# Kernel optimization log

Measured on AMD Instinct MI355X. Metric: run time of the kernel, lower is better.

The kernel has to match this reference:

```python
import jax, jax.numpy as jnp
import numpy as np

WD, WH, WW = 2, 7, 7
N = WD * WH * WW          # 98 tokens per window
DIM = 128
HEADS = 4
HEAD_DIM = DIM // HEADS   # 32
B_ = 2048                 # num_windows * batch
NW = 64                   # windows per image (mask leading dim)
TABLE = (2 * WD - 1) * (2 * WH - 1) * (2 * WW - 1)  # 507


def _relative_position_index():
    coords = np.stack(np.meshgrid(np.arange(WD), np.arange(WH), np.arange(WW), indexing='ij'))
    flat = coords.reshape(3, -1)                     # [3, N]
    rel = flat[:, :, None] - flat[:, None, :]        # [3, N, N]
    rel = rel.transpose(1, 2, 0).copy()              # [N, N, 3]
    rel[:, :, 0] += WD - 1
    rel[:, :, 1] += WH - 1
    rel[:, :, 2] += WW - 1
    rel[:, :, 0] *= (2 * WH - 1) * (2 * WW - 1)
    rel[:, :, 1] *= 2 * WW - 1
    return rel.sum(-1).astype(np.int32)             # [N, N]


def setup_inputs() -> dict:
    key = jax.random.key(0)
    ks = jax.random.split(key, 6)
    x = jax.random.normal(ks[0], (B_, N, DIM), dtype=jnp.float32)
    mask = jax.random.normal(ks[1], (NW, N, N), dtype=jnp.float32)
    qkv_w = jax.random.normal(ks[2], (3 * DIM, DIM), dtype=jnp.float32) * 0.02
    qkv_b = jnp.zeros((3 * DIM,), dtype=jnp.float32)
    proj_w = jax.random.normal(ks[3], (DIM, DIM), dtype=jnp.float32) * 0.02
    proj_b = jnp.zeros((DIM,), dtype=jnp.float32)
    bias_table = jax.random.normal(ks[4], (TABLE, HEADS), dtype=jnp.float32) * 0.02
    rel_idx = jnp.asarray(_relative_position_index())
    return {"x": x, "mask": mask, "qkv_w": qkv_w, "qkv_b": qkv_b,
            "proj_w": proj_w, "proj_b": proj_b, "bias_table": bias_table,
            "rel_idx": rel_idx}


def reference(x, mask, qkv_w, qkv_b, proj_w, proj_b, bias_table, rel_idx):
    b, n, c = x.shape
    hd = c // HEADS
    scale = hd ** -0.5
    qkv = x @ qkv_w.T + qkv_b                          # [B_, N, 3C]
    qkv = qkv.reshape(b, n, 3, HEADS, hd)
    qkv = jnp.transpose(qkv, (2, 0, 3, 1, 4))          # [3, B_, H, N, hd]
    q, k, v = qkv[0], qkv[1], qkv[2]
    attn = jnp.einsum('bhnd,bhmd->bhnm', q * scale, k)  # [B_, H, N, N]
    # gathered relative position bias
    bias = bias_table[rel_idx.reshape(-1)].reshape(n, n, HEADS)
    bias = jnp.transpose(bias, (2, 0, 1))               # [H, N, N]
    attn = attn + bias[None]
    nw = mask.shape[0]
    attn = attn.reshape(b // nw, nw, HEADS, n, n) + mask[None, :, None]
    attn = jax.nn.softmax(attn.reshape(b, HEADS, n, n), axis=-1)
    out = jnp.einsum('bhnm,bhmd->bnhd', attn, v).reshape(b, n, c)
    out = out @ proj_w.T + proj_b
    return out
```

## Files before the change

### kernel.cpp

```cpp
#include <hip/hip_runtime.h>
#include <stdint.h>

#define NTOK 98
#define DIM 128
#define HEADS 4
#define HD 32
#define BWIN 2048
#define NW 64
#define SCALE 0.17677669529663687f
#define QSTR 40
#define VSTR 104

typedef __bf16 bf16_t;
typedef bf16_t bf16x8 __attribute__((ext_vector_type(8)));
typedef float f32x4 __attribute__((ext_vector_type(4)));
typedef unsigned short u16;
typedef unsigned int u32;
typedef unsigned long long u64;

__device__ __forceinline__ u16 f2bf(float f) {
    union { bf16_t h; u16 u; } v; v.h = (bf16_t)f; return v.u;
}
__device__ __forceinline__ float bf2f(u16 b) {
    union { u16 u; bf16_t h; } v; v.u = b; return (float)v.h;
}

__global__ void k0_prep(const float* __restrict__ qkv_w, const float* __restrict__ proj_w,
                        const float* __restrict__ mask,
                        const float* __restrict__ bias_table, const int* __restrict__ rel_idx,
                        u16* __restrict__ qkvw_bf, u16* __restrict__ pw_bf,
                        u16* __restrict__ mbT)
{
    int t = blockIdx.x * 256 + threadIdx.x;
    if (t < 49152) {
        qkvw_bf[t] = f2bf(qkv_w[t]);
    } else if (t < 65536) {
        int r = t - 49152;
        pw_bf[r] = f2bf(proj_w[r]);
    } else {
        int r = t - 65536;
        int w    = r / 50176;
        int rem  = r - w * 50176;
        int hh   = rem / 12544;
        int rem2 = rem - hh * 12544;
        int i    = rem2 >> 7;
        int c    = rem2 & 127;
        int l16  = c >> 3;
        int njp  = c & 7;
        int j    = njp * 16 + l16;
        float val = 0.f;
        if (njp < 7 && j < NTOK)
            val = mask[w * 9604 + i * NTOK + j] + bias_table[rel_idx[i * NTOK + j] * HEADS + hh];
        mbT[r] = f2bf(val);
    }
}

__global__ __launch_bounds__(512, 2) void k_fused(
    const float* __restrict__ x, const u16* __restrict__ qkvw_bf,
    const float* __restrict__ qkv_b, const u16* __restrict__ mbT,
    const u16* __restrict__ pw_bf, const float* __restrict__ proj_b,
    float* __restrict__ out)
{
    __shared__ __align__(16) u16 XO[98 * 136];
    __shared__ __align__(16) u16 qLs[HEADS][98 * QSTR];
    __shared__ __align__(16) u16 kLs[HEADS][98 * QSTR];
    __shared__ __align__(16) u16 vLs[HEADS][HD * VSTR];
    __shared__ __align__(16) u16 Pscr[8][16 * VSTR];
    __shared__ float qkvb_l[384];
    __shared__ float projb_l[128];

    const int b    = blockIdx.x;
    const int tid  = threadIdx.x;
    const int wave = tid >> 6;
    const int lane = tid & 63;
    const int l16  = lane & 15;
    const int quad = lane >> 4;

    if (tid < 384) qkvb_l[tid] = qkv_b[tid];
    else projb_l[tid - 384] = proj_b[tid - 384];

    const float* xb = x + (size_t)b * (NTOK * DIM);
    for (int idx = tid; idx < (NTOK * DIM / 4); idx += 512) {
        int row = idx >> 5;
        int c4  = idx & 31;
        const float4 v = reinterpret_cast<const float4*>(xb)[idx];
        u64 pack = (u64)f2bf(v.x) | ((u64)f2bf(v.y) << 16) |
                   ((u64)f2bf(v.z) << 32) | ((u64)f2bf(v.w) << 48);
        *reinterpret_cast<u64*>(&XO[row * 136 + c4 * 4]) = pack;
    }
    __syncthreads();

    {
        const int u0 = wave * 3 - ((wave > 5) ? (wave - 5) : 0);
        const int u1 = u0 + ((wave < 5) ? 3 : 2);
        for (int np = 0; np < 4; ++np) {
            int cached = -1;
            bf16x8 Bf[2][4];
            for (int u = u0; u < u1; ++u) {
                const int part = u / 7;
                const int mt   = u - part * 7;
                if (part != cached) {
                    const u16* wp = qkvw_bf + (size_t)part * DIM * DIM;
#pragma unroll
                    for (int half = 0; half < 2; ++half)
#pragma unroll
                        for (int ks = 0; ks < 4; ++ks)
                            Bf[half][ks] = *reinterpret_cast<const bf16x8*>(
                                wp + ((np * 2 + half) * 16 + l16) * DIM + quad * 8 + ks * 32);
                    cached = part;
                }
                int arow = mt * 16 + l16;
                if (arow > 97) arow = 97;
                f32x4 acc0 = {0.f, 0.f, 0.f, 0.f};
                f32x4 acc1 = {0.f, 0.f, 0.f, 0.f};
#pragma unroll
                for (int ks = 0; ks < 4; ++ks) {
                    bf16x8 a = *reinterpret_cast<const bf16x8*>(
                        &XO[arow * 136 + quad * 8 + ks * 32]);
                    acc0 = __builtin_amdgcn_mfma_f32_16x16x32_bf16(a, Bf[0][ks], acc0, 0, 0, 0);
                    acc1 = __builtin_amdgcn_mfma_f32_16x16x32_bf16(a, Bf[1][ks], acc1, 0, 0, 0);
                }
                const int tokb = mt * 16 + quad * 4;
#pragma unroll
                for (int half = 0; half < 2; ++half) {
                    const f32x4& acc = half ? acc1 : acc0;
                    int col = (np * 2 + half) * 16 + l16;
                    int h   = col >> 5;
                    int d   = col & 31;
                    float cb = qkvb_l[part * DIM + col];
                    if (part == 0) {
#pragma unroll
                        for (int reg = 0; reg < 4; ++reg) {
                            int tok = tokb + reg;
                            if (tok < NTOK)
                                qLs[h][tok * QSTR + d] = f2bf((acc[reg] + cb) * SCALE);
                        }
                    } else if (part == 1) {
#pragma unroll
                        for (int reg = 0; reg < 4; ++reg) {
                            int tok = tokb + reg;
                            if (tok < NTOK)
                                kLs[h][tok * QSTR + d] = f2bf(acc[reg] + cb);
                        }
                    } else {
                        u16* vrow = &vLs[h][d * VSTR];
                        if (tokb + 3 <= 97) {
                            u64 pack = 0;
#pragma unroll
                            for (int reg = 0; reg < 4; ++reg)
                                pack |= ((u64)f2bf(acc[reg] + cb)) << (16 * reg);
                            *reinterpret_cast<u64*>(&vrow[tokb]) = pack;
                        } else if (tokb <= 97) {
                            u32 pack = (u32)f2bf(acc[0] + cb) | ((u32)f2bf(acc[1] + cb) << 16);
                            *reinterpret_cast<u32*>(&vrow[tokb]) = pack;
                        }
                    }
                }
            }
        }
    }
    __syncthreads();

    {
        const int h   = wave >> 1;
        const int mlo = (wave & 1) ? 4 : 0;
        const int mhi = (wave & 1) ? 7 : 4;
        const u16* qh  = &qLs[h][0];
        const u16* kh  = &kLs[h][0];
        const u16* vh  = &vLs[h][0];
        const u16* mbtp = mbT + ((size_t)((b & (NW - 1)) * HEADS + h)) * (NTOK * 128);
        u16* ps = &Pscr[wave][0];

        bf16x8 kf[7];
#pragma unroll
        for (int nj = 0; nj < 7; ++nj)
            kf[nj] = *reinterpret_cast<const bf16x8*>(&kh[(nj * 16 + l16) * QSTR + quad * 8]);

        for (int mt = mlo; mt < mhi; ++mt) {
            bf16x8 mrows[4];
#pragma unroll
            for (int reg = 0; reg < 4; ++reg) {
                int i  = mt * 16 + quad * 4 + reg;
                int ic = (i > 97) ? 97 : i;
                mrows[reg] = *reinterpret_cast<const bf16x8*>(&mbtp[ic * 128 + l16 * 8]);
            }
            bf16x8 qf = *reinterpret_cast<const bf16x8*>(&qh[(mt * 16 + l16) * QSTR + quad * 8]);
            f32x4 sacc[7];
#pragma unroll
            for (int nj = 0; nj < 7; ++nj) {
                f32x4 z = {0.f, 0.f, 0.f, 0.f};
                sacc[nj] = __builtin_amdgcn_mfma_f32_16x16x32_bf16(qf, kf[nj], z, 0, 0, 0);
            }
#pragma unroll
            for (int reg = 0; reg < 4; ++reg) {
                int i = mt * 16 + quad * 4 + reg;
                bool irow = (i < NTOK);
                float s[7];
#pragma unroll
                for (int nj = 0; nj < 7; ++nj) {
                    int j = nj * 16 + l16;
                    float val = -1e30f;
                    if (irow && j < NTOK)
                        val = sacc[nj][reg] + (float)mrows[reg][nj];
                    s[nj] = val;
                }
                float mx = s[0];
#pragma unroll
                for (int nj = 1; nj < 7; ++nj) mx = fmaxf(mx, s[nj]);
#pragma unroll
                for (int off = 1; off < 16; off <<= 1) mx = fmaxf(mx, __shfl_xor(mx, off));
                float p[7];
                float lsum = 0.f;
#pragma unroll
                for (int nj = 0; nj < 7; ++nj) {
                    float pv = (s[nj] > -1e29f) ? __expf(s[nj] - mx) : 0.f;
                    p[nj] = pv;
                    lsum += pv;
                }
#pragma unroll
                for (int off = 1; off < 16; off <<= 1) lsum += __shfl_xor(lsum, off);
                float rinv = 1.f / ((lsum > 0.f) ? lsum : 1.f);
#pragma unroll
                for (int nj = 0; nj < 7; ++nj) {
                    int j = nj * 16 + l16;
                    if (irow && j < NTOK)
                        ps[(quad * 4 + reg) * VSTR + j] = f2bf(p[nj] * rinv);
                }
            }
            bf16x8 pf[3];
#pragma unroll
            for (int ks = 0; ks < 3; ++ks)
                pf[ks] = *reinterpret_cast<const bf16x8*>(&ps[l16 * VSTR + quad * 8 + ks * 32]);
#pragma unroll
            for (int nt = 0; nt < 2; ++nt) {
                f32x4 oacc = {0.f, 0.f, 0.f, 0.f};
#pragma unroll
                for (int ks = 0; ks < 3; ++ks) {
                    bf16x8 vf = *reinterpret_cast<const bf16x8*>(
                        &vh[(nt * 16 + l16) * VSTR + quad * 8 + ks * 32]);
                    oacc = __builtin_amdgcn_mfma_f32_16x16x32_bf16(pf[ks], vf, oacc, 0, 0, 0);
                }
                int d = nt * 16 + l16;
                float v96 = bf2f(vh[d * VSTR + 96]);
                float v97 = bf2f(vh[d * VSTR + 97]);
#pragma unroll
                for (int reg = 0; reg < 4; ++reg) {
                    int i = mt * 16 + quad * 4 + reg;
                    if (i < NTOK) {
                        float p96 = bf2f(ps[(quad * 4 + reg) * VSTR + 96]);
                        float p97 = bf2f(ps[(quad * 4 + reg) * VSTR + 97]);
                        XO[i * 136 + h * HD + d] = f2bf(oacc[reg] + p96 * v96 + p97 * v97);
                    }
                }
            }
        }
    }
    __syncthreads();

    {
        const int nt = wave;
        bf16x8 bw[4];
#pragma unroll
        for (int ks = 0; ks < 4; ++ks)
            bw[ks] = *reinterpret_cast<const bf16x8*>(
                pw_bf + (nt * 16 + l16) * DIM + quad * 8 + ks * 32);
        const int col = nt * 16 + l16;
        const float pb = projb_l[col];
        for (int mt = 0; mt < 7; ++mt) {
            int arow = mt * 16 + l16;
            if (arow > 97) arow = 97;
            f32x4 acc = {0.f, 0.f, 0.f, 0.f};
#pragma unroll
            for (int ks = 0; ks < 4; ++ks) {
                bf16x8 a = *reinterpret_cast<const bf16x8*>(
                    &XO[arow * 136 + quad * 8 + ks * 32]);
                acc = __builtin_amdgcn_mfma_f32_16x16x32_bf16(a, bw[ks], acc, 0, 0, 0);
            }
#pragma unroll
            for (int reg = 0; reg < 4; ++reg) {
                int row = mt * 16 + quad * 4 + reg;
                if (row < NTOK)
                    out[((size_t)b * NTOK + row) * DIM + col] = acc[reg] + pb;
            }
        }
    }
}

extern "C" void kernel_launch(void* const* d_in, const int* in_sizes, int n_in,
                              void* d_out, int out_size, void* d_ws, size_t ws_size,
                              hipStream_t stream)
{
    const float* x       = (const float*)d_in[0];
    const float* mask    = (const float*)d_in[1];
    const float* qkv_w   = (const float*)d_in[2];
    const float* qkv_b   = (const float*)d_in[3];
    const float* proj_w  = (const float*)d_in[4];
    const float* proj_b  = (const float*)d_in[5];
    const float* bias_tb = (const float*)d_in[6];
    const int*   rel_idx = (const int*)d_in[7];
    float* out = (float*)d_out;

    char* ws = (char*)d_ws;
    u16* qkvw_bf = (u16*)(ws + 0);
    u16* pw_bf   = (u16*)(ws + 98304);
    u16* mbT     = (u16*)(ws + 131072);

    k0_prep<<<12800, 256, 0, stream>>>(qkv_w, proj_w, mask, bias_tb, rel_idx,
                                       qkvw_bf, pw_bf, mbT);
    k_fused<<<BWIN, 512, 0, stream>>>(x, qkvw_bf, qkv_b, mbT, pw_bf, proj_b, out);
}
```

Baseline: 403.9 us.

## Split fused window attention into per-head attention kernel plus separate projection kernel

The single per-window kernel is replaced by a per-(window, head) attention kernel with 256 threads and smaller shared memory. It reads x directly from global memory, converts it to bf16 in registers, and writes the bf16 head outputs to a workspace buffer. A second kernel then performs the output projection. The aim is higher occupancy and more blocks in flight. The cost is that x is re-read once per head and there is an extra global round trip for the attention output.

```diff
diff --git a/kernel.cpp b/kernel.cpp
--- a/kernel.cpp
+++ b/kernel.cpp
@@ -55,20 +55,204 @@
     }
 }
 
-__global__ __launch_bounds__(512, 2) void k_fused(
+__global__ __launch_bounds__(256, 4) void k_attn(
     const float* __restrict__ x, const u16* __restrict__ qkvw_bf,
     const float* __restrict__ qkv_b, const u16* __restrict__ mbT,
-    const u16* __restrict__ pw_bf, const float* __restrict__ proj_b,
-    float* __restrict__ out)
+    u16* __restrict__ OG)
 {
-    __shared__ __align__(16) u16 XO[98 * 136];
-    __shared__ __align__(16) u16 qLs[HEADS][98 * QSTR];
-    __shared__ __align__(16) u16 kLs[HEADS][98 * QSTR];
-    __shared__ __align__(16) u16 vLs[HEADS][HD * VSTR];
-    __shared__ __align__(16) u16 Pscr[8][16 * VSTR];
-    __shared__ float qkvb_l[384];
-    __shared__ float projb_l[128];
-
+    __shared__ __align__(16) u16 qL[NTOK * QSTR];
+    __shared__ __align__(16) u16 kL[NTOK * QSTR];
+    __shared__ __align__(16) u16 vL[HD * VSTR];
+    __shared__ __align__(16) u16 Pscr[4][16 * VSTR];
+
+    const int bh   = (blockIdx.x & 7) * 1024 + (blockIdx.x >> 3);
+    const int b    = bh >> 2;
+    const int h    = bh & 3;
+    const int tid  = threadIdx.x;
+    const int wave = tid >> 6;
+    const int lane = tid & 63;
+    const int l16  = lane & 15;
+    const int quad = lane >> 4;
+
+    const float* xb = x + (size_t)b * (NTOK * DIM);
+
+    {
+        const int u0 = (wave * 21) >> 2;
+        const int u1 = ((wave + 1) * 21) >> 2;
+        int cached = -1;
+        bf16x8 Bf[2][4];
+        float  cb[2];
+        for (int u = u0; u < u1; ++u) {
+            const int part = u / 7;
+            const int mt   = u - part * 7;
+            if (part != cached) {
+                const u16* wp = qkvw_bf + (size_t)part * DIM * DIM;
+#pragma unroll
+                for (int nt2 = 0; nt2 < 2; ++nt2) {
+                    const int col = h * HD + nt2 * 16 + l16;
+#pragma unroll
+                    for (int ks = 0; ks < 4; ++ks)
+                        Bf[nt2][ks] = *reinterpret_cast<const bf16x8*>(
+                            wp + col * DIM + quad * 8 + ks * 32);
+                    cb[nt2] = qkv_b[part * DIM + col];
+                }
+                cached = part;
+            }
+            int arow = mt * 16 + l16;
+            if (arow > 97) arow = 97;
+            bf16x8 af[4];
+#pragma unroll
+            for (int ks = 0; ks < 4; ++ks) {
+                const float* xr = xb + arow * DIM + quad * 8 + ks * 32;
+                const float4 a0 = *reinterpret_cast<const float4*>(xr);
+                const float4 a1 = *reinterpret_cast<const float4*>(xr + 4);
+                bf16x8 a;
+                a[0] = (bf16_t)a0.x; a[1] = (bf16_t)a0.y; a[2] = (bf16_t)a0.z; a[3] = (bf16_t)a0.w;
+                a[4] = (bf16_t)a1.x; a[5] = (bf16_t)a1.y; a[6] = (bf16_t)a1.z; a[7] = (bf16_t)a1.w;
+                af[ks] = a;
+            }
+            f32x4 acc0 = {0.f, 0.f, 0.f, 0.f};
+            f32x4 acc1 = {0.f, 0.f, 0.f, 0.f};
+#pragma unroll
+            for (int ks = 0; ks < 4; ++ks) {
+                acc0 = __builtin_amdgcn_mfma_f32_16x16x32_bf16(af[ks], Bf[0][ks], acc0, 0, 0, 0);
+                acc1 = __builtin_amdgcn_mfma_f32_16x16x32_bf16(af[ks], Bf[1][ks], acc1, 0, 0, 0);
+            }
+            const int tokb = mt * 16 + quad * 4;
+#pragma unroll
+            for (int nt2 = 0; nt2 < 2; ++nt2) {
+                const f32x4& acc = nt2 ? acc1 : acc0;
+                const int d = nt2 * 16 + l16;
+                const float cbv = cb[nt2];
+                if (part == 0) {
+#pragma unroll
+                    for (int reg = 0; reg < 4; ++reg) {
+                        int tok = tokb + reg;
+                        if (tok < NTOK)
+                            qL[tok * QSTR + d] = f2bf((acc[reg] + cbv) * SCALE);
+                    }
+                } else if (part == 1) {
+#pragma unroll
+                    for (int reg = 0; reg < 4; ++reg) {
+                        int tok = tokb + reg;
+                        if (tok < NTOK)
+                            kL[tok * QSTR + d] = f2bf(acc[reg] + cbv);
+                    }
+                } else {
+                    u16* vrow = &vL[d * VSTR];
+                    if (tokb + 3 <= 97) {
+                        u64 pack = 0;
+#pragma unroll
+                        for (int reg = 0; reg < 4; ++reg)
+                            pack |= ((u64)f2bf(acc[reg] + cbv)) << (16 * reg);
+                        *reinterpret_cast<u64*>(&vrow[tokb]) = pack;
+                    } else if (tokb <= 97) {
+                        u32 pack = (u32)f2bf(acc[0] + cbv) | ((u32)f2bf(acc[1] + cbv) << 16);
+                        *reinterpret_cast<u32*>(&vrow[tokb]) = pack;
+                    }
+                }
+            }
+        }
+    }
+    __syncthreads();
+
+    {
+        const u16* mbtp = mbT + ((size_t)((b & (NW - 1)) * HEADS + h)) * (NTOK * 128);
+        u16* ps = &Pscr[wave][0];
+
+        bf16x8 kf[7];
+#pragma unroll
+        for (int nj = 0; nj < 7; ++nj)
+            kf[nj] = *reinterpret_cast<const bf16x8*>(&kL[(nj * 16 + l16) * QSTR + quad * 8]);
+
+        for (int mi = 0; mi < 2; ++mi) {
+            const int mt = wave + mi * 4;
+            if (mt > 6) break;
+            bf16x8 mrows[4];
+#pragma unroll
+            for (int reg = 0; reg < 4; ++reg) {
+                int i  = mt * 16 + quad * 4 + reg;
+                int ic = (i > 97) ? 97 : i;
+                mrows[reg] = *reinterpret_cast<const bf16x8*>(&mbtp[ic * 128 + l16 * 8]);
+            }
+            bf16x8 qf = *reinterpret_cast<const bf16x8*>(&qL[(mt * 16 + l16) * QSTR + quad * 8]);
+            f32x4 sacc[7];
+#pragma unroll
+            for (int nj = 0; nj < 7; ++nj) {
+                f32x4 z = {0.f, 0.f, 0.f, 0.f};
+                sacc[nj] = __builtin_amdgcn_mfma_f32_16x16x32_bf16(qf, kf[nj], z, 0, 0, 0);
+            }
+#pragma unroll
+            for (int reg = 0; reg < 4; ++reg) {
+                int i = mt * 16 + quad * 4 + reg;
+                bool irow = (i < NTOK);
+                float s[7];
+#pragma unroll
+                for (int nj = 0; nj < 7; ++nj) {
+                    int j = nj * 16 + l16;
+                    float val = -1e30f;
+                    if (irow && j < NTOK)
+                        val = sacc[nj][reg] + (float)mrows[reg][nj];
+                    s[nj] = val;
+                }
+                float mx = s[0];
+#pragma unroll
+                for (int nj = 1; nj < 7; ++nj) mx = fmaxf(mx, s[nj]);
+#pragma unroll
+                for (int off = 1; off < 16; off <<= 1) mx = fmaxf(mx, __shfl_xor(mx, off));
+                float p[7];
+                float lsum = 0.f;
+#pragma unroll
+                for (int nj = 0; nj < 7; ++nj) {
+                    float pv = (s[nj] > -1e29f) ? __expf(s[nj] - mx) : 0.f;
+                    p[nj] = pv;
+                    lsum += pv;
+                }
+#pragma unroll
+                for (int off = 1; off < 16; off <<= 1) lsum += __shfl_xor(lsum, off);
+                float rinv = 1.f / ((lsum > 0.f) ? lsum : 1.f);
+#pragma unroll
+                for (int nj = 0; nj < 7; ++nj) {
+                    int j = nj * 16 + l16;
+                    if (irow && j < NTOK)
+                        ps[(quad * 4 + reg) * VSTR + j] = f2bf(p[nj] * rinv);
+                }
+            }
+            bf16x8 pf[3];
+#pragma unroll
+            for (int ks = 0; ks < 3; ++ks)
+                pf[ks] = *reinterpret_cast<const bf16x8*>(&ps[l16 * VSTR + quad * 8 + ks * 32]);
+#pragma unroll
+            for (int nt = 0; nt < 2; ++nt) {
+                f32x4 oacc = {0.f, 0.f, 0.f, 0.f};
+#pragma unroll
+                for (int ks = 0; ks < 3; ++ks) {
+                    bf16x8 vf = *reinterpret_cast<const bf16x8*>(
+                        &vL[(nt * 16 + l16) * VSTR + quad * 8 + ks * 32]);
+                    oacc = __builtin_amdgcn_mfma_f32_16x16x32_bf16(pf[ks], vf, oacc, 0, 0, 0);
+                }
+                int d = nt * 16 + l16;
+                float v96 = bf2f(vL[d * VSTR + 96]);
+                float v97 = bf2f(vL[d * VSTR + 97]);
+#pragma unroll
+                for (int reg = 0; reg < 4; ++reg) {
+                    int i = mt * 16 + quad * 4 + reg;
+                    if (i < NTOK) {
+                        float p96 = bf2f(ps[(quad * 4 + reg) * VSTR + 96]);
+                        float p97 = bf2f(ps[(quad * 4 + reg) * VSTR + 97]);
+                        OG[((size_t)b * NTOK + i) * DIM + h * HD + d] =
+                            f2bf(oacc[reg] + p96 * v96 + p97 * v97);
+                    }
+                }
+            }
+        }
+    }
+}
+
+__global__ __launch_bounds__(256, 4) void k_proj(
+    const u16* __restrict__ OG, const u16* __restrict__ pw_bf,
+    const float* __restrict__ proj_b, float* __restrict__ out)
+{
     const int b    = blockIdx.x;
     const int tid  = threadIdx.x;
     const int wave = tid >> 6;
@@ -76,211 +260,41 @@
     const int l16  = lane & 15;
     const int quad = lane >> 4;
 
-    if (tid < 384) qkvb_l[tid] = qkv_b[tid];
-    else projb_l[tid - 384] = proj_b[tid - 384];
-
-    const float* xb = x + (size_t)b * (NTOK * DIM);
-    for (int idx = tid; idx < (NTOK * DIM / 4); idx += 512) {
-        int row = idx >> 5;
-        int c4  = idx & 31;
-        const float4 v = reinterpret_cast<const float4*>(xb)[idx];
-        u64 pack = (u64)f2bf(v.x) | ((u64)f2bf(v.y) << 16) |
-                   ((u64)f2bf(v.z) << 32) | ((u64)f2bf(v.w) << 48);
-        *reinterpret_cast<u64*>(&XO[row * 136 + c4 * 4]) = pack;
-    }
-    __syncthreads();
-
-    {
-        const int u0 = wave * 3 - ((wave > 5) ? (wave - 5) : 0);
-        const int u1 = u0 + ((wave < 5) ? 3 : 2);
-        for (int np = 0; np < 4; ++np) {
-            int cached = -1;
-            bf16x8 Bf[2][4];
-            for (int u = u0; u < u1; ++u) {
-                const int part = u / 7;
-                const int mt   = u - part * 7;
-                if (part != cached) {
-                    const u16* wp = qkvw_bf + (size_t)part * DIM * DIM;
-#pragma unroll
-                    for (int half = 0; half < 2; ++half)
-#pragma unroll
-                        for (int ks = 0; ks < 4; ++ks)
-                            Bf[half][ks] = *reinterpret_cast<const bf16x8*>(
-                                wp + ((np * 2 + half) * 16 + l16) * DIM + quad * 8 + ks * 32);
-                    cached = part;
-                }
-                int arow = mt * 16 + l16;
-                if (arow > 97) arow = 97;
-                f32x4 acc0 = {0.f, 0.f, 0.f, 0.f};
-                f32x4 acc1 = {0.f, 0.f, 0.f, 0.f};
-#pragma unroll
-                for (int ks = 0; ks < 4; ++ks) {
-                    bf16x8 a = *reinterpret_cast<const bf16x8*>(
-                        &XO[arow * 136 + quad * 8 + ks * 32]);
-                    acc0 = __builtin_amdgcn_mfma_f32_16x16x32_bf16(a, Bf[0][ks], acc0, 0, 0, 0);
-                    acc1 = __builtin_amdgcn_mfma_f32_16x16x32_bf16(a, Bf[1][ks], acc1, 0, 0, 0);
-                }
-                const int tokb = mt * 16 + quad * 4;
-#pragma unroll
-                for (int half = 0; half < 2; ++half) {
-                    const f32x4& acc = half ? acc1 : acc0;
-                    int col = (np * 2 + half) * 16 + l16;
-                    int h   = col >> 5;
-                    int d   = col & 31;
-                    float cb = qkvb_l[part * DIM + col];
-                    if (part == 0) {
-#pragma unroll
-                        for (int reg = 0; reg < 4; ++reg) {
-                            int tok = tokb + reg;
-                            if (tok < NTOK)
-                                qLs[h][tok * QSTR + d] = f2bf((acc[reg] + cb) * SCALE);
-                        }
-                    } else if (part == 1) {
-#pragma unroll
-                        for (int reg = 0; reg < 4; ++reg) {
-                            int tok = tokb + reg;
-                            if (tok < NTOK)
-                                kLs[h][tok * QSTR + d] = f2bf(acc[reg] + cb);
-                        }
-                    } else {
-                        u16* vrow = &vLs[h][d * VSTR];
-                        if (tokb + 3 <= 97) {
-                            u64 pack = 0;
-#pragma unroll
-                            for (int reg = 0; reg < 4; ++reg)
-                                pack |= ((u64)f2bf(acc[reg] + cb)) << (16 * reg);
-                            *reinterpret_cast<u64*>(&vrow[tokb]) = pack;
-                        } else if (tokb <= 97) {
-                            u32 pack = (u32)f2bf(acc[0] + cb) | ((u32)f2bf(acc[1] + cb) << 16);
-                            *reinterpret_cast<u32*>(&vrow[tokb]) = pack;
-                        }
-                    }
-                }
-            }
+    bf16x8 bw[2][4];
+    float  pb[2];
+#pragma unroll
+    for (int nt2 = 0; nt2 < 2; ++nt2) {
+        const int col = (wave * 2 + nt2) * 16 + l16;
+#pragma unroll
+        for (int ks = 0; ks < 4; ++ks)
+            bw[nt2][ks] = *reinterpret_cast<const bf16x8*>(
+                pw_bf + col * DIM + quad * 8 + ks * 32);
+        pb[nt2] = proj_b[col];
+    }
+    const u16* ob = OG + (size_t)b * (NTOK * DIM);
+    for (int mt = 0; mt < 7; ++mt) {
+        int arow = mt * 16 + l16;
+        if (arow > 97) arow = 97;
+        bf16x8 af[4];
+#pragma unroll
+        for (int ks = 0; ks < 4; ++ks)
+            af[ks] = *reinterpret_cast<const bf16x8*>(ob + arow * DIM + quad * 8 + ks * 32);
+        f32x4 acc0 = {0.f, 0.f, 0.f, 0.f};
+        f32x4 acc1 = {0.f, 0.f, 0.f, 0.f};
+#pragma unroll
+        for (int ks = 0; ks < 4; ++ks) {
+            acc0 = __builtin_amdgcn_mfma_f32_16x16x32_bf16(af[ks], bw[0][ks], acc0, 0, 0, 0);
+            acc1 = __builtin_amdgcn_mfma_f32_16x16x32_bf16(af[ks], bw[1][ks], acc1, 0, 0, 0);
         }
-    }
-    __syncthreads();
-
-    {
-        const int h   = wave >> 1;
-        const int mlo = (wave & 1) ? 4 : 0;
-        const int mhi = (wave & 1) ? 7 : 4;
-        const u16* qh  = &qLs[h][0];
-        const u16* kh  = &kLs[h][0];
-        const u16* vh  = &vLs[h][0];
-        const u16* mbtp = mbT + ((size_t)((b & (NW - 1)) * HEADS + h)) * (NTOK * 128);
-        u16* ps = &Pscr[wave][0];
-
-        bf16x8 kf[7];
-#pragma unroll
-        for (int nj = 0; nj < 7; ++nj)
-            kf[nj] = *reinterpret_cast<const bf16x8*>(&kh[(nj * 16 + l16) * QSTR + quad * 8]);
-
-        for (int mt = mlo; mt < mhi; ++mt) {
-            bf16x8 mrows[4];
-#pragma unroll
-            for (int reg = 0; reg < 4; ++reg) {
-                int i  = mt * 16 + quad * 4 + reg;
-                int ic = (i > 97) ? 97 : i;
-                mrows[reg] = *reinterpret_cast<const bf16x8*>(&mbtp[ic * 128 + l16 * 8]);
-            }
-            bf16x8 qf = *reinterpret_cast<const bf16x8*>(&qh[(mt * 16 + l16) * QSTR + quad * 8]);
-            f32x4 sacc[7];
-#pragma unroll
-            for (int nj = 0; nj < 7; ++nj) {
-                f32x4 z = {0.f, 0.f, 0.f, 0.f};
-                sacc[nj] = __builtin_amdgcn_mfma_f32_16x16x32_bf16(qf, kf[nj], z, 0, 0, 0);
-            }
-#pragma unroll
-            for (int reg = 0; reg < 4; ++reg) {
-                int i = mt * 16 + quad * 4 + reg;
-                bool irow = (i < NTOK);
-                float s[7];
-#pragma unroll
-                for (int nj = 0; nj < 7; ++nj) {
-                    int j = nj * 16 + l16;
-                    float val = -1e30f;
-                    if (irow && j < NTOK)
-                        val = sacc[nj][reg] + (float)mrows[reg][nj];
-                    s[nj] = val;
-                }
-                float mx = s[0];
-#pragma unroll
-                for (int nj = 1; nj < 7; ++nj) mx = fmaxf(mx, s[nj]);
-#pragma unroll
-                for (int off = 1; off < 16; off <<= 1) mx = fmaxf(mx, __shfl_xor(mx, off));
-                float p[7];
-                float lsum = 0.f;
-#pragma unroll
-                for (int nj = 0; nj < 7; ++nj) {
-                    float pv = (s[nj] > -1e29f) ? __expf(s[nj] - mx) : 0.f;
-                    p[nj] = pv;
-                    lsum += pv;
-                }
-#pragma unroll
-                for (int off = 1; off < 16; off <<= 1) lsum += __shfl_xor(lsum, off);
-                float rinv = 1.f / ((lsum > 0.f) ? lsum : 1.f);
-#pragma unroll
-                for (int nj = 0; nj < 7; ++nj) {
-                    int j = nj * 16 + l16;
-                    if (irow && j < NTOK)
-                        ps[(quad * 4 + reg) * VSTR + j] = f2bf(p[nj] * rinv);
-                }
-            }
-            bf16x8 pf[3];
-#pragma unroll
-            for (int ks = 0; ks < 3; ++ks)
-                pf[ks] = *reinterpret_cast<const bf16x8*>(&ps[l16 * VSTR + quad * 8 + ks * 32]);
-#pragma unroll
-            for (int nt = 0; nt < 2; ++nt) {
-                f32x4 oacc = {0.f, 0.f, 0.f, 0.f};
-#pragma unroll
-                for (int ks = 0; ks < 3; ++ks) {
-                    bf16x8 vf = *reinterpret_cast<const bf16x8*>(
-                        &vh[(nt * 16 + l16) * VSTR + quad * 8 + ks * 32]);
-                    oacc = __builtin_amdgcn_mfma_f32_16x16x32_bf16(pf[ks], vf, oacc, 0, 0, 0);
-                }
-                int d = nt * 16 + l16;
-                float v96 = bf2f(vh[d * VSTR + 96]);
-                float v97 = bf2f(vh[d * VSTR + 97]);
-#pragma unroll
-                for (int reg = 0; reg < 4; ++reg) {
-                    int i = mt * 16 + quad * 4 + reg;
-                    if (i < NTOK) {
-                        float p96 = bf2f(ps[(quad * 4 + reg) * VSTR + 96]);
-                        float p97 = bf2f(ps[(quad * 4 + reg) * VSTR + 97]);
-                        XO[i * 136 + h * HD + d] = f2bf(oacc[reg] + p96 * v96 + p97 * v97);
-                    }
-                }
-            }
-        }
-    }
-    __syncthreads();
-
-    {
-        const int nt = wave;
-        bf16x8 bw[4];
-#pragma unroll
-        for (int ks = 0; ks < 4; ++ks)
-            bw[ks] = *reinterpret_cast<const bf16x8*>(
-                pw_bf + (nt * 16 + l16) * DIM + quad * 8 + ks * 32);
-        const int col = nt * 16 + l16;
-        const float pb = projb_l[col];
-        for (int mt = 0; mt < 7; ++mt) {
-            int arow = mt * 16 + l16;
-            if (arow > 97) arow = 97;
-            f32x4 acc = {0.f, 0.f, 0.f, 0.f};
-#pragma unroll
-            for (int ks = 0; ks < 4; ++ks) {
-                bf16x8 a = *reinterpret_cast<const bf16x8*>(
-                    &XO[arow * 136 + quad * 8 + ks * 32]);
-                acc = __builtin_amdgcn_mfma_f32_16x16x32_bf16(a, bw[ks], acc, 0, 0, 0);
-            }
+#pragma unroll
+        for (int nt2 = 0; nt2 < 2; ++nt2) {
+            const f32x4& acc = nt2 ? acc1 : acc0;
+            const int col = (wave * 2 + nt2) * 16 + l16;
 #pragma unroll
             for (int reg = 0; reg < 4; ++reg) {
                 int row = mt * 16 + quad * 4 + reg;
                 if (row < NTOK)
-                    out[((size_t)b * NTOK + row) * DIM + col] = acc[reg] + pb;
+                    out[((size_t)b * NTOK + row) * DIM + col] = acc[reg] + pb[nt2];
             }
         }
     }
@@ -304,8 +318,10 @@
     u16* qkvw_bf = (u16*)(ws + 0);
     u16* pw_bf   = (u16*)(ws + 98304);
     u16* mbT     = (u16*)(ws + 131072);
+    u16* OG      = (u16*)(ws + 6553600);
 
     k0_prep<<<12800, 256, 0, stream>>>(qkv_w, proj_w, mask, bias_tb, rel_idx,
                                        qkvw_bf, pw_bf, mbT);
-    k_fused<<<BWIN, 512, 0, stream>>>(x, qkvw_bf, qkv_b, mbT, pw_bf, proj_b, out);
-}
+    k_attn<<<BWIN * HEADS, 256, 0, stream>>>(x, qkvw_bf, qkv_b, mbT, OG);
+    k_proj<<<BWIN, 256, 0, stream>>>(OG, pw_bf, proj_b, out);
+}
```

Result: faster. 389.4 us (-3.6%).
